# Performance work log

Hardware: AMD Instinct MI355X
Metric: run time of the kernel (lower is better)

## Reference

```python
import jax, jax.numpy as jnp
import numpy as np

K = 32
EPS = 1e-16


def setup_inputs() -> dict:
    key = jax.random.key(0)
    k1, k2, k3 = jax.random.split(key, 3)
    N_l, N_h, D, F = 8192, 32768, 3, 128
    x = jax.random.normal(k1, (N_l, F), dtype=jnp.float32)
    pos_l = jax.random.normal(k2, (N_l, D), dtype=jnp.float32)
    pos_h = jax.random.normal(k3, (N_h, D), dtype=jnp.float32)
    return {"x": x, "pos_l": pos_l, "pos_h": pos_h}


def reference(x, pos_l, pos_h):
    # Squared pairwise distances [N_h, N_l] via ||h||^2 - 2 h.l + ||l||^2
    h2 = jnp.sum(pos_h * pos_h, axis=1, keepdims=True)        # [N_h, 1]
    l2 = jnp.sum(pos_l * pos_l, axis=1)                        # [N_l]
    d2 = h2 - 2.0 * (pos_h @ pos_l.T) + l2[None, :]            # [N_h, N_l]
    # k nearest source points per target point
    neg_d2k, idx = jax.lax.top_k(-d2, K)                       # [N_h, K]
    d2k = -neg_d2k
    # Inverse squared-distance weights (torch_geometric: 1/clamp(d2, min=1e-16))
    w = 1.0 / jnp.maximum(d2k, EPS)                            # [N_h, K]
    xk = x[idx]                                                # [N_h, K, F]
    y = jnp.einsum('nk,nkf->nf', w, xk) / jnp.sum(w, axis=1, keepdims=True)
    return y
```

## Files before the change

kernel.cpp:

```cpp
#include <hip/hip_runtime.h>
#include <stdint.h>

#define NL      8192
#define NH      32768
#define FDIM    128
#define KSEL    32
#define QPW     8
#define NWAVES  4
#define BLOCK   (NWAVES * 64)
#define QPB     (NWAVES * QPW)
#define BUFCAP  256
#define NGROUP  (NL / 64)
#define NCELL   4096
#define TSCAN   4
#define MAXPASS 6

__device__ __forceinline__ int imin(int a, int b) { return a < b ? a : b; }
__device__ __forceinline__ int imax(int a, int b) { return a > b ? a : b; }

__device__ __forceinline__ uint32_t spread3(uint32_t x) {
    x &= 0xFu;
    x = (x | (x << 16)) & 0x030000FFu;
    x = (x | (x << 8))  & 0x0300F00Fu;
    x = (x | (x << 4))  & 0x030C30C3u;
    x = (x | (x << 2))  & 0x09249249u;
    return x;
}
__device__ __forceinline__ int cell_of(float px, float py, float pz) {
    int ix = (int)floorf((px + 4.0f) * 2.0f);
    int iy = (int)floorf((py + 4.0f) * 2.0f);
    int iz = (int)floorf((pz + 4.0f) * 2.0f);
    ix = imin(imax(ix, 0), 15); iy = imin(imax(iy, 0), 15); iz = imin(imax(iz, 0), 15);
    return (int)(spread3((uint32_t)ix) | (spread3((uint32_t)iy) << 1) | (spread3((uint32_t)iz) << 2));
}

__global__ void k_cell_count(const float* __restrict__ pos_l, int* __restrict__ hist) {
    const int i = blockIdx.x * 256 + threadIdx.x;
    if (i >= NL) return;
    const int c = cell_of(pos_l[i * 3 + 0], pos_l[i * 3 + 1], pos_l[i * 3 + 2]);
    atomicAdd(&hist[c], 1);
}

__global__ void k_cell_scan(const int* __restrict__ hist, int* __restrict__ cursor) {
    __shared__ int part[256];
    __shared__ int partpref[256];
    const int tid = threadIdx.x;
    int loc[16];
    int s = 0;
#pragma unroll
    for (int i = 0; i < 16; ++i) { loc[i] = s; s += hist[tid * 16 + i]; }
    part[tid] = s;
    __syncthreads();
    if (tid == 0) {
        int a = 0;
        for (int t = 0; t < 256; ++t) { partpref[t] = a; a += part[t]; }
    }
    __syncthreads();
    const int b = partpref[tid];
#pragma unroll
    for (int i = 0; i < 16; ++i) cursor[tid * 16 + i] = b + loc[i];
}

__global__ void k_scatter(const float* __restrict__ pos_l, int* __restrict__ cursor,
                          float4* __restrict__ sorted, int* __restrict__ oidx) {
    const int i = blockIdx.x * 256 + threadIdx.x;
    if (i >= NL) return;
    const float px = pos_l[i * 3 + 0];
    const float py = pos_l[i * 3 + 1];
    const float pz = pos_l[i * 3 + 2];
    const int c = cell_of(px, py, pz);
    const int pos = atomicAdd(&cursor[c], 1);
    sorted[pos] = make_float4(px, py, pz, px * px + py * py + pz * pz);
    oidx[pos] = i;
}

__global__ void k_spheres(const float4* __restrict__ sorted, float4* __restrict__ spheres) {
    const int g = blockIdx.x;
    const int lane = threadIdx.x;
    const float4 p = sorted[g * 64 + lane];
    float sx = p.x, sy = p.y, sz = p.z;
#pragma unroll
    for (int j = 32; j >= 1; j >>= 1) {
        sx += __shfl_xor(sx, j); sy += __shfl_xor(sy, j); sz += __shfl_xor(sz, j);
    }
    const float cx = sx * (1.0f / 64.0f), cy = sy * (1.0f / 64.0f), cz = sz * (1.0f / 64.0f);
    const float dx = p.x - cx, dy = p.y - cy, dz = p.z - cz;
    float d2 = dx * dx + dy * dy + dz * dz;
#pragma unroll
    for (int j = 32; j >= 1; j >>= 1) d2 = fmaxf(d2, __shfl_xor(d2, j));
    if (lane == 0) spheres[g] = make_float4(cx, cy, cz, sqrtf(d2) + 1e-3f);
}

__global__ __launch_bounds__(BLOCK, 4)
void knn_interp_kernel(const float* __restrict__ x,
                       const float* __restrict__ pos_h,
                       const float4* __restrict__ sorted,
                       const float4* __restrict__ spheres,
                       const int* __restrict__ oidx,
                       float* __restrict__ out)
{
    __shared__ float4   s_grp[NGROUP];
    __shared__ unsigned long long s_surv[NWAVES][QPW][2];
    __shared__ uint16_t s_idx[QPB][BUFCAP];
    __shared__ float    s_w[QPB][KSEL];
    __shared__ int      s_wi[QPB][KSEL];

    const int tid   = threadIdx.x;
    const int lane  = tid & 63;
    const int wid   = tid >> 6;
    const int qbase = blockIdx.x * QPB + wid * QPW;
    const unsigned long long mlt = (1ull << lane) - 1ull;

    if (tid < NGROUP) s_grp[tid] = spheres[tid];
    __syncthreads();

    const float4 cA = s_grp[lane];
    const float4 cB = s_grp[lane + 64];

    float qx[QPW], qy[QPW], qz[QPW], h2q[QPW], tauD[QPW];

#pragma unroll
    for (int q = 0; q < QPW; ++q) {
        const int gq = qbase + q;
        qx[q] = pos_h[gq * 3 + 0];
        qy[q] = pos_h[gq * 3 + 1];
        qz[q] = pos_h[gq * 3 + 2];
        h2q[q] = fmaf(qx[q], qx[q], fmaf(qy[q], qy[q], qz[q] * qz[q]));

        const float dAx = qx[q] - cA.x, dAy = qy[q] - cA.y, dAz = qz[q] - cA.z;
        const float dA  = fmaf(dAx, dAx, fmaf(dAy, dAy, dAz * dAz));
        const float dBx = qx[q] - cB.x, dBy = qy[q] - cB.y, dBz = qz[q] - cB.z;
        const float dB  = fmaf(dBx, dBx, fmaf(dBy, dBy, dBz * dBz));

        int kA = (int)((__float_as_uint(dA) & 0xFFFFFF00u) | (uint32_t)lane);
        int kB = (int)((__float_as_uint(dB) & 0xFFFFFF00u) | (uint32_t)(lane + 64));

        int gsel[TSCAN];
#pragma unroll
        for (int t = 0; t < TSCAN; ++t) {
            int m = imin(kA, kB);
#pragma unroll
            for (int j = 1; j <= 32; j <<= 1) m = imin(m, __shfl_xor(m, j));
            gsel[t] = m & 0xFF;
            if (kA == m) kA = 0x7FFFFFFF;
            if (kB == m) kB = 0x7FFFFFFF;
        }

        float dmin = INFINITY;
#pragma unroll
        for (int t = 0; t < TSCAN; ++t) {
            const float4 p = sorted[(gsel[t] << 6) + lane];
            const float s = fmaf(qx[q], p.x, fmaf(qy[q], p.y, qz[q] * p.z));
            dmin = fminf(dmin, fmaf(-2.0f, s, p.w));
        }
        float v = dmin;
#pragma unroll
        for (int k = 2; k <= 64; k <<= 1) {
#pragma unroll
            for (int j = k >> 1; j >= 1; j >>= 1) {
                const float o     = __shfl_xor(v, j);
                const bool  up    = ((lane & k) == 0);
                const bool  lower = ((lane & j) == 0);
                v = (lower == up) ? fminf(v, o) : fmaxf(v, o);
            }
        }
        const float tau = __shfl(v, 31) + 1e-4f;
        tauD[q] = tau;

        const float st = sqrtf(fmaxf(tau + h2q[q], 0.0f)) + 1e-3f;
        const float tA = st + cA.w, tB = st + cB.w;
        const unsigned long long bA = __ballot(dA <= tA * tA);
        const unsigned long long bB = __ballot(dB <= tB * tB);
        if (lane == 0) { s_surv[wid][q][0] = bA; s_surv[wid][q][1] = bB; }
    }

#pragma unroll 1
    for (int q = 0; q < QPW; ++q) {
        const int QQ = wid * QPW + q;
        const int gq = qbase + q;
        float tau = tauD[q];
        int M = 0;

#pragma unroll 1
        for (int pass = 0; pass < MAXPASS; ++pass) {
            M = 0;
#pragma unroll 1
            for (int h = 0; h < 2; ++h) {
                unsigned long long mm = s_surv[wid][q][h];
                while (mm) {
                    const int g = (h << 6) + __builtin_ctzll(mm);
                    mm &= mm - 1;
                    const float4 p = sorted[(g << 6) + lane];
                    const float s = fmaf(qx[q], p.x, fmaf(qy[q], p.y, qz[q] * p.z));
                    const float D = fmaf(-2.0f, s, p.w);
                    const bool hit = (D <= tau);
                    const unsigned long long b = __ballot(hit);
                    if (b) {
                        const int o = M + (int)__popcll(b & mlt);
                        if (hit && o < BUFCAP) s_idx[QQ][o] = (uint16_t)((g << 6) + lane);
                        M += (int)__popcll(b);
                    }
                }
            }
            if (M <= BUFCAP) break;
            int kk[4];
#pragma unroll
            for (int r = 0; r < 4; ++r) {
                const int idx = (int)s_idx[QQ][64 * r + lane];
                const float4 c = sorted[idx];
                const float s = fmaf(qx[q], c.x, fmaf(qy[q], c.y, qz[q] * c.z));
                const float d2 = fmaxf(fmaf(-2.0f, s, c.w) + h2q[q], 0.0f);
                kk[r] = __float_as_int(d2);
            }
            int lo = 0, hi = 0x7F800000;
            while (lo < hi) {
                const int mid = (int)(((unsigned)lo + (unsigned)hi) >> 1);
                int cnt = 0;
#pragma unroll
                for (int r = 0; r < 4; ++r)
                    cnt += (int)__popcll(__ballot(kk[r] <= mid));
                if (cnt >= KSEL) hi = mid; else lo = mid + 1;
            }
            tau = __int_as_float(lo) - h2q[q] + 1e-4f;
        }
        if (M > BUFCAP) M = BUFCAP;

        const double ax = (double)qx[q], ay = (double)qy[q], az = (double)qz[q];
        if (M <= 128) {
            const int i0 = (2 * lane     < M) ? (int)s_idx[QQ][2 * lane]     : -1;
            const int i1 = (2 * lane + 1 < M) ? (int)s_idx[QQ][2 * lane + 1] : -1;
            float f0 = INFINITY, f1 = INFINITY;
            if (i0 >= 0) {
                const float4 c = sorted[i0];
                const double dx = (double)c.x - ax, dy = (double)c.y - ay, dz = (double)c.z - az;
                f0 = (float)(dx * dx + dy * dy + dz * dz);
            }
            if (i1 >= 0) {
                const float4 c = sorted[i1];
                const double dx = (double)c.x - ax, dy = (double)c.y - ay, dz = (double)c.z - az;
                f1 = (float)(dx * dx + dy * dy + dz * dz);
            }
            int v0 = __float_as_int(f0);
            int v1 = __float_as_int(f1);
#pragma unroll
            for (int k = 2; k <= 128; k <<= 1) {
                const bool up = ((lane & (k >> 1)) == 0);
#pragma unroll
                for (int j = k >> 1; j >= 2; j >>= 1) {
                    const int  xo    = j >> 1;
                    const bool lower = ((lane & xo) == 0);
                    const int o0 = __shfl_xor(v0, xo);
                    const int o1 = __shfl_xor(v1, xo);
                    v0 = (lower == up) ? imin(v0, o0) : imax(v0, o0);
                    v1 = (lower == up) ? imin(v1, o1) : imax(v1, o1);
                }
                const int mn = imin(v0, v1), mx = imax(v0, v1);
                v0 = up ? mn : mx;
                v1 = up ? mx : mn;
            }
            const int tau32 = __shfl(v1, 15);
            const bool a0 = (i0 >= 0) && (__float_as_int(f0) <= tau32);
            const bool a1 = (i1 >= 0) && (__float_as_int(f1) <= tau32);
            const unsigned long long b0 = __ballot(a0);
            const unsigned long long b1 = __ballot(a1);
            const int base = (int)__popcll(b0 & mlt) + (int)__popcll(b1 & mlt);
            const int p0 = base;
            const int p1 = base + (a0 ? 1 : 0);
            if (a0 && p0 < KSEL) { s_w[QQ][p0] = 1.0f / fmaxf(f0, 1e-16f); s_wi[QQ][p0] = oidx[i0]; }
            if (a1 && p1 < KSEL) { s_w[QQ][p1] = 1.0f / fmaxf(f1, 1e-16f); s_wi[QQ][p1] = oidx[i1]; }
        } else {
            int ii[4]; float ff[4]; int kk_[4];
#pragma unroll
            for (int r = 0; r < 4; ++r) {
                const int e = 4 * lane + r;
                ii[r] = (e < M) ? (int)s_idx[QQ][e] : -1;
                ff[r] = INFINITY;
                if (ii[r] >= 0) {
                    const float4 c = sorted[ii[r]];
                    const double dx = (double)c.x - ax, dy = (double)c.y - ay, dz = (double)c.z - az;
                    ff[r] = (float)(dx * dx + dy * dy + dz * dz);
                }
                kk_[r] = __float_as_int(ff[r]);
            }
            int lo = 0, hi = 0x7F800000;
            while (lo < hi) {
                const int mid = (int)(((unsigned)lo + (unsigned)hi) >> 1);
                int cnt = 0;
#pragma unroll
                for (int r = 0; r < 4; ++r)
                    cnt += (int)__popcll(__ballot(ii[r] >= 0 && kk_[r] <= mid));
                if (cnt >= KSEL) hi = mid; else lo = mid + 1;
            }
            const int tau32 = lo;
            bool a[4]; unsigned long long b[4];
#pragma unroll
            for (int r = 0; r < 4; ++r) {
                a[r] = (ii[r] >= 0) && (kk_[r] <= tau32);
                b[r] = __ballot(a[r]);
            }
            int base = 0;
#pragma unroll
            for (int r = 0; r < 4; ++r) base += (int)__popcll(b[r] & mlt);
            int pref = 0;
#pragma unroll
            for (int r = 0; r < 4; ++r) {
                const int p = base + pref;
                if (a[r] && p < KSEL) { s_w[QQ][p] = 1.0f / fmaxf(ff[r], 1e-16f); s_wi[QQ][p] = oidx[ii[r]]; }
                pref += (a[r] ? 1 : 0);
            }
        }

        float acc0 = 0.0f, acc1 = 0.0f, wsum = 0.0f;
#pragma unroll 8
        for (int t = 0; t < KSEL; ++t) {
            const float w   = s_w[QQ][t];
            const int   idx = s_wi[QQ][t];
            const float* row = x + (size_t)idx * FDIM;
            acc0 = fmaf(w, row[lane], acc0);
            acc1 = fmaf(w, row[lane + 64], acc1);
            wsum += w;
        }
        const float invw = 1.0f / wsum;
        out[(size_t)gq * FDIM + lane]      = acc0 * invw;
        out[(size_t)gq * FDIM + 64 + lane] = acc1 * invw;
    }
}

extern "C" void kernel_launch(void* const* d_in, const int* in_sizes, int n_in,
                              void* d_out, int out_size, void* d_ws, size_t ws_size,
                              hipStream_t stream) {
    const float* x     = (const float*)d_in[0];
    const float* pos_l = (const float*)d_in[1];
    const float* pos_h = (const float*)d_in[2];
    float* out = (float*)d_out;

    char* ws = (char*)d_ws;
    int*    hist    = (int*)(ws + 0);
    int*    cursor  = (int*)(ws + 16384);
    float4* spheres = (float4*)(ws + 32768);
    float4* sorted  = (float4*)(ws + 65536);
    int*    oidx    = (int*)(ws + 65536 + 131072);

    hipMemsetAsync(hist, 0, NCELL * sizeof(int), stream);
    hipLaunchKernelGGL(k_cell_count, dim3(NL / 256), dim3(256), 0, stream, pos_l, hist);
    hipLaunchKernelGGL(k_cell_scan, dim3(1), dim3(256), 0, stream, hist, cursor);
    hipLaunchKernelGGL(k_scatter, dim3(NL / 256), dim3(256), 0, stream, pos_l, cursor, sorted, oidx);
    hipLaunchKernelGGL(k_spheres, dim3(NGROUP), dim3(64), 0, stream, sorted, spheres);
    hipLaunchKernelGGL(knn_interp_kernel, dim3(NH / QPB), dim3(BLOCK), 0, stream,
                       x, pos_h, sorted, spheres, oidx, out);
}
```

Before: 220.9 us.

## Fuse preprocessing into one kernel, shrink blocks, use ballot rank-select and prefetch

The memset and four preprocessing kernels (histogram, scan, scatter, sphere bounds) are merged into one single-block kernel that does its counting sort in shared memory, removing several launches. The main kernel moves to smaller blocks (2 waves, 4 queries each) with a higher occupancy hint, and reads sphere data straight from global memory instead of staging it in LDS. Bitonic sorts and iterative min-extraction are replaced by a ballot-based binary-search rank select. The initial threshold now takes the 32nd smallest of 64 lane minima rather than the sorted value at lane 31. The candidate scan loop prefetches the next group's points to hide load latency. The single-block preprocess serialises that stage on one CU, and the binary search adds about 31 ballot rounds per selection.

```diff
diff --git a/kernel.cpp b/kernel.cpp
--- a/kernel.cpp
+++ b/kernel.cpp
@@ -5,8 +5,8 @@
 #define NH      32768
 #define FDIM    128
 #define KSEL    32
-#define QPW     8
-#define NWAVES  4
+#define QPW     4
+#define NWAVES  2
 #define BLOCK   (NWAVES * 64)
 #define QPB     (NWAVES * QPW)
 #define BUFCAP  256
@@ -14,9 +14,42 @@
 #define NCELL   4096
 #define TSCAN   4
 #define MAXPASS 6
+#define PRE_T   1024
 
 __device__ __forceinline__ int imin(int a, int b) { return a < b ? a : b; }
 __device__ __forceinline__ int imax(int a, int b) { return a > b ? a : b; }
+
+__device__ __forceinline__ int rank_select1(int k0, int rank) {
+    unsigned lo = 0u, hi = 0x7F800000u;
+    while (lo < hi) {
+        const int mid = (int)((lo + hi) >> 1);
+        const int cnt = (int)__popcll(__ballot(k0 <= mid));
+        if (cnt >= rank) hi = (unsigned)mid; else lo = (unsigned)mid + 1u;
+    }
+    return (int)lo;
+}
+__device__ __forceinline__ int rank_select2(int k0, int k1, int rank) {
+    unsigned lo = 0u, hi = 0x7F800000u;
+    while (lo < hi) {
+        const int mid = (int)((lo + hi) >> 1);
+        const int cnt = (int)__popcll(__ballot(k0 <= mid))
+                      + (int)__popcll(__ballot(k1 <= mid));
+        if (cnt >= rank) hi = (unsigned)mid; else lo = (unsigned)mid + 1u;
+    }
+    return (int)lo;
+}
+__device__ __forceinline__ int rank_select4(const int* k, int rank) {
+    unsigned lo = 0u, hi = 0x7F800000u;
+    while (lo < hi) {
+        const int mid = (int)((lo + hi) >> 1);
+        int cnt = 0;
+#pragma unroll
+        for (int r = 0; r < 4; ++r)
+            cnt += (int)__popcll(__ballot(k[r] <= mid));
+        if (cnt >= rank) hi = (unsigned)mid; else lo = (unsigned)mid + 1u;
+    }
+    return (int)lo;
+}
 
 __device__ __forceinline__ uint32_t spread3(uint32_t x) {
     x &= 0xFu;
@@ -34,64 +67,78 @@
     return (int)(spread3((uint32_t)ix) | (spread3((uint32_t)iy) << 1) | (spread3((uint32_t)iz) << 2));
 }
 
-__global__ void k_cell_count(const float* __restrict__ pos_l, int* __restrict__ hist) {
-    const int i = blockIdx.x * 256 + threadIdx.x;
-    if (i >= NL) return;
-    const int c = cell_of(pos_l[i * 3 + 0], pos_l[i * 3 + 1], pos_l[i * 3 + 2]);
-    atomicAdd(&hist[c], 1);
-}
-
-__global__ void k_cell_scan(const int* __restrict__ hist, int* __restrict__ cursor) {
-    __shared__ int part[256];
-    __shared__ int partpref[256];
-    const int tid = threadIdx.x;
-    int loc[16];
-    int s = 0;
-#pragma unroll
-    for (int i = 0; i < 16; ++i) { loc[i] = s; s += hist[tid * 16 + i]; }
-    part[tid] = s;
-    __syncthreads();
-    if (tid == 0) {
-        int a = 0;
-        for (int t = 0; t < 256; ++t) { partpref[t] = a; a += part[t]; }
-    }
-    __syncthreads();
-    const int b = partpref[tid];
-#pragma unroll
-    for (int i = 0; i < 16; ++i) cursor[tid * 16 + i] = b + loc[i];
-}
-
-__global__ void k_scatter(const float* __restrict__ pos_l, int* __restrict__ cursor,
-                          float4* __restrict__ sorted, int* __restrict__ oidx) {
-    const int i = blockIdx.x * 256 + threadIdx.x;
-    if (i >= NL) return;
-    const float px = pos_l[i * 3 + 0];
-    const float py = pos_l[i * 3 + 1];
-    const float pz = pos_l[i * 3 + 2];
-    const int c = cell_of(px, py, pz);
-    const int pos = atomicAdd(&cursor[c], 1);
-    sorted[pos] = make_float4(px, py, pz, px * px + py * py + pz * pz);
-    oidx[pos] = i;
-}
-
-__global__ void k_spheres(const float4* __restrict__ sorted, float4* __restrict__ spheres) {
-    const int g = blockIdx.x;
-    const int lane = threadIdx.x;
-    const float4 p = sorted[g * 64 + lane];
-    float sx = p.x, sy = p.y, sz = p.z;
-#pragma unroll
-    for (int j = 32; j >= 1; j >>= 1) {
-        sx += __shfl_xor(sx, j); sy += __shfl_xor(sy, j); sz += __shfl_xor(sz, j);
-    }
-    const float cx = sx * (1.0f / 64.0f), cy = sy * (1.0f / 64.0f), cz = sz * (1.0f / 64.0f);
-    const float dx = p.x - cx, dy = p.y - cy, dz = p.z - cz;
-    float d2 = dx * dx + dy * dy + dz * dz;
-#pragma unroll
-    for (int j = 32; j >= 1; j >>= 1) d2 = fmaxf(d2, __shfl_xor(d2, j));
-    if (lane == 0) spheres[g] = make_float4(cx, cy, cz, sqrtf(d2) + 1e-3f);
-}
-
-__global__ __launch_bounds__(BLOCK, 4)
+__global__ __launch_bounds__(PRE_T)
+void k_preprocess(const float* __restrict__ pos_l,
+                  float4* __restrict__ sorted, int* __restrict__ oidx,
+                  float4* __restrict__ spheres)
+{
+    __shared__ int hist[NCELL];
+    __shared__ int wpart[PRE_T / 64];
+    const int tid  = threadIdx.x;
+    const int lane = tid & 63;
+    const int wv   = tid >> 6;
+
+    for (int i = tid; i < NCELL; i += PRE_T) hist[i] = 0;
+    __syncthreads();
+
+    int cc[8]; float px[8], py[8], pz[8];
+#pragma unroll
+    for (int r = 0; r < 8; ++r) {
+        const int i = r * PRE_T + tid;
+        px[r] = pos_l[i * 3 + 0];
+        py[r] = pos_l[i * 3 + 1];
+        pz[r] = pos_l[i * 3 + 2];
+        cc[r] = cell_of(px[r], py[r], pz[r]);
+        atomicAdd(&hist[cc[r]], 1);
+    }
+    __syncthreads();
+
+    int loc[4]; int ts = 0;
+#pragma unroll
+    for (int i = 0; i < 4; ++i) { loc[i] = ts; ts += hist[tid * 4 + i]; }
+    int incl = ts;
+#pragma unroll
+    for (int d = 1; d < 64; d <<= 1) {
+        const int t = __shfl_up(incl, d);
+        if (lane >= d) incl += t;
+    }
+    if (lane == 63) wpart[wv] = incl;
+    __syncthreads();
+    int base = 0;
+    for (int j = 0; j < wv; ++j) base += wpart[j];
+    const int texcl = base + incl - ts;
+#pragma unroll
+    for (int i = 0; i < 4; ++i) hist[tid * 4 + i] = texcl + loc[i];
+    __syncthreads();
+
+#pragma unroll
+    for (int r = 0; r < 8; ++r) {
+        const int pos = atomicAdd(&hist[cc[r]], 1);
+        sorted[pos] = make_float4(px[r], py[r], pz[r],
+                                  fmaf(px[r], px[r], fmaf(py[r], py[r], pz[r] * pz[r])));
+        oidx[pos] = r * PRE_T + tid;
+    }
+    __syncthreads();
+
+#pragma unroll
+    for (int r = 0; r < NGROUP / (PRE_T / 64); ++r) {
+        const int g = wv * (NGROUP / (PRE_T / 64)) + r;
+        const float4 p = sorted[g * 64 + lane];
+        float sx = p.x, sy = p.y, sz = p.z;
+#pragma unroll
+        for (int j = 32; j >= 1; j >>= 1) {
+            sx += __shfl_xor(sx, j); sy += __shfl_xor(sy, j); sz += __shfl_xor(sz, j);
+        }
+        const float cx = sx * (1.0f / 64.0f), cy = sy * (1.0f / 64.0f), cz = sz * (1.0f / 64.0f);
+        const float dx = p.x - cx, dy = p.y - cy, dz = p.z - cz;
+        float d2 = fmaf(dx, dx, fmaf(dy, dy, dz * dz));
+#pragma unroll
+        for (int j = 32; j >= 1; j >>= 1) d2 = fmaxf(d2, __shfl_xor(d2, j));
+        if (lane == 0) spheres[g] = make_float4(cx, cy, cz, sqrtf(d2) + 1e-3f);
+    }
+}
+
+__global__ __launch_bounds__(BLOCK, 6)
 void knn_interp_kernel(const float* __restrict__ x,
                        const float* __restrict__ pos_h,
                        const float4* __restrict__ sorted,
@@ -99,11 +146,10 @@
                        const int* __restrict__ oidx,
                        float* __restrict__ out)
 {
-    __shared__ float4   s_grp[NGROUP];
-    __shared__ unsigned long long s_surv[NWAVES][QPW][2];
     __shared__ uint16_t s_idx[QPB][BUFCAP];
     __shared__ float    s_w[QPB][KSEL];
     __shared__ int      s_wi[QPB][KSEL];
+    __shared__ unsigned long long s_surv[NWAVES][QPW][2];
 
     const int tid   = threadIdx.x;
     const int lane  = tid & 63;
@@ -111,63 +157,47 @@
     const int qbase = blockIdx.x * QPB + wid * QPW;
     const unsigned long long mlt = (1ull << lane) - 1ull;
 
-    if (tid < NGROUP) s_grp[tid] = spheres[tid];
-    __syncthreads();
-
-    const float4 cA = s_grp[lane];
-    const float4 cB = s_grp[lane + 64];
+    const float4 cA = spheres[lane];
+    const float4 cB = spheres[lane + 64];
 
     float qx[QPW], qy[QPW], qz[QPW], h2q[QPW], tauD[QPW];
 
 #pragma unroll
     for (int q = 0; q < QPW; ++q) {
         const int gq = qbase + q;
-        qx[q] = pos_h[gq * 3 + 0];
-        qy[q] = pos_h[gq * 3 + 1];
-        qz[q] = pos_h[gq * 3 + 2];
-        h2q[q] = fmaf(qx[q], qx[q], fmaf(qy[q], qy[q], qz[q] * qz[q]));
-
-        const float dAx = qx[q] - cA.x, dAy = qy[q] - cA.y, dAz = qz[q] - cA.z;
+        const float ax = pos_h[gq * 3 + 0];
+        const float ay = pos_h[gq * 3 + 1];
+        const float az = pos_h[gq * 3 + 2];
+        qx[q] = ax; qy[q] = ay; qz[q] = az;
+        const float h2 = fmaf(ax, ax, fmaf(ay, ay, az * az));
+        h2q[q] = h2;
+
+        const float dAx = ax - cA.x, dAy = ay - cA.y, dAz = az - cA.z;
         const float dA  = fmaf(dAx, dAx, fmaf(dAy, dAy, dAz * dAz));
-        const float dBx = qx[q] - cB.x, dBy = qy[q] - cB.y, dBz = qz[q] - cB.z;
+        const float dBx = ax - cB.x, dBy = ay - cB.y, dBz = az - cB.z;
         const float dB  = fmaf(dBx, dBx, fmaf(dBy, dBy, dBz * dBz));
 
-        int kA = (int)((__float_as_uint(dA) & 0xFFFFFF00u) | (uint32_t)lane);
-        int kB = (int)((__float_as_uint(dB) & 0xFFFFFF00u) | (uint32_t)(lane + 64));
-
-        int gsel[TSCAN];
-#pragma unroll
+        const int kA = (int)((__float_as_uint(dA) & 0xFFFFFF00u) | (uint32_t)lane);
+        const int kB = (int)((__float_as_uint(dB) & 0xFFFFFF00u) | (uint32_t)(lane + 64));
+        const int t4 = rank_select2(kA, kB, TSCAN);
+        unsigned long long gm0 = __ballot(kA <= t4);
+        unsigned long long gm1 = __ballot(kB <= t4);
+
+        float dmin = INFINITY;
+#pragma unroll 1
         for (int t = 0; t < TSCAN; ++t) {
-            int m = imin(kA, kB);
-#pragma unroll
-            for (int j = 1; j <= 32; j <<= 1) m = imin(m, __shfl_xor(m, j));
-            gsel[t] = m & 0xFF;
-            if (kA == m) kA = 0x7FFFFFFF;
-            if (kB == m) kB = 0x7FFFFFFF;
-        }
-
-        float dmin = INFINITY;
-#pragma unroll
-        for (int t = 0; t < TSCAN; ++t) {
-            const float4 p = sorted[(gsel[t] << 6) + lane];
-            const float s = fmaf(qx[q], p.x, fmaf(qy[q], p.y, qz[q] * p.z));
+            int g;
+            if (gm0) { g = __builtin_ctzll(gm0); gm0 &= gm0 - 1ull; }
+            else     { g = 64 + __builtin_ctzll(gm1); gm1 &= gm1 - 1ull; }
+            const float4 p = sorted[(g << 6) + lane];
+            const float s = fmaf(ax, p.x, fmaf(ay, p.y, az * p.z));
             dmin = fminf(dmin, fmaf(-2.0f, s, p.w));
         }
-        float v = dmin;
-#pragma unroll
-        for (int k = 2; k <= 64; k <<= 1) {
-#pragma unroll
-            for (int j = k >> 1; j >= 1; j >>= 1) {
-                const float o     = __shfl_xor(v, j);
-                const bool  up    = ((lane & k) == 0);
-                const bool  lower = ((lane & j) == 0);
-                v = (lower == up) ? fminf(v, o) : fmaxf(v, o);
-            }
-        }
-        const float tau = __shfl(v, 31) + 1e-4f;
-        tauD[q] = tau;
-
-        const float st = sqrtf(fmaxf(tau + h2q[q], 0.0f)) + 1e-3f;
+        const float d2min = fmaxf(dmin + h2, 0.0f);
+        const int t32 = rank_select1(__float_as_int(d2min), KSEL);
+        const float tau_d2 = __int_as_float(t32) + 1e-4f;
+        tauD[q] = tau_d2 - h2;
+        const float st = sqrtf(tau_d2) + 1e-3f;
         const float tA = st + cA.w, tB = st + cB.w;
         const unsigned long long bA = __ballot(dA <= tA * tA);
         const unsigned long long bB = __ballot(dB <= tB * tB);
@@ -178,29 +208,38 @@
     for (int q = 0; q < QPW; ++q) {
         const int QQ = wid * QPW + q;
         const int gq = qbase + q;
+        const float ax = qx[q], ay = qy[q], az = qz[q];
         float tau = tauD[q];
         int M = 0;
 
 #pragma unroll 1
         for (int pass = 0; pass < MAXPASS; ++pass) {
             M = 0;
+            unsigned long long m0 = s_surv[wid][q][0];
+            unsigned long long m1 = s_surv[wid][q][1];
+            int g_cur = -1;
+            if (m0)      { g_cur = __builtin_ctzll(m0); m0 &= m0 - 1ull; }
+            else if (m1) { g_cur = 64 + __builtin_ctzll(m1); m1 &= m1 - 1ull; }
+            float4 pc = make_float4(0, 0, 0, 0);
+            if (g_cur >= 0) pc = sorted[(g_cur << 6) + lane];
 #pragma unroll 1
-            for (int h = 0; h < 2; ++h) {
-                unsigned long long mm = s_surv[wid][q][h];
-                while (mm) {
-                    const int g = (h << 6) + __builtin_ctzll(mm);
-                    mm &= mm - 1;
-                    const float4 p = sorted[(g << 6) + lane];
-                    const float s = fmaf(qx[q], p.x, fmaf(qy[q], p.y, qz[q] * p.z));
-                    const float D = fmaf(-2.0f, s, p.w);
-                    const bool hit = (D <= tau);
-                    const unsigned long long b = __ballot(hit);
-                    if (b) {
-                        const int o = M + (int)__popcll(b & mlt);
-                        if (hit && o < BUFCAP) s_idx[QQ][o] = (uint16_t)((g << 6) + lane);
-                        M += (int)__popcll(b);
-                    }
+            while (g_cur >= 0) {
+                int g_nxt = -1;
+                if (m0)      { g_nxt = __builtin_ctzll(m0); m0 &= m0 - 1ull; }
+                else if (m1) { g_nxt = 64 + __builtin_ctzll(m1); m1 &= m1 - 1ull; }
+                float4 pn = pc;
+                if (g_nxt >= 0) pn = sorted[(g_nxt << 6) + lane];
+
+                const float s = fmaf(ax, pc.x, fmaf(ay, pc.y, az * pc.z));
+                const float D = fmaf(-2.0f, s, pc.w);
+                const bool hit = (D <= tau);
+                const unsigned long long b = __ballot(hit);
+                if (b) {
+                    const int o = M + (int)__popcll(b & mlt);
+                    if (hit && o < BUFCAP) s_idx[QQ][o] = (uint16_t)((g_cur << 6) + lane);
+                    M += (int)__popcll(b);
                 }
+                g_cur = g_nxt; pc = pn;
             }
             if (M <= BUFCAP) break;
             int kk[4];
@@ -208,59 +247,34 @@
             for (int r = 0; r < 4; ++r) {
                 const int idx = (int)s_idx[QQ][64 * r + lane];
                 const float4 c = sorted[idx];
-                const float s = fmaf(qx[q], c.x, fmaf(qy[q], c.y, qz[q] * c.z));
+                const float s = fmaf(ax, c.x, fmaf(ay, c.y, az * c.z));
                 const float d2 = fmaxf(fmaf(-2.0f, s, c.w) + h2q[q], 0.0f);
                 kk[r] = __float_as_int(d2);
             }
-            int lo = 0, hi = 0x7F800000;
-            while (lo < hi) {
-                const int mid = (int)(((unsigned)lo + (unsigned)hi) >> 1);
-                int cnt = 0;
-#pragma unroll
-                for (int r = 0; r < 4; ++r)
-                    cnt += (int)__popcll(__ballot(kk[r] <= mid));
-                if (cnt >= KSEL) hi = mid; else lo = mid + 1;
-            }
-            tau = __int_as_float(lo) - h2q[q] + 1e-4f;
+            const int tk = rank_select4(kk, KSEL);
+            tau = __int_as_float(tk) + 1e-4f - h2q[q];
         }
         if (M > BUFCAP) M = BUFCAP;
 
-        const double ax = (double)qx[q], ay = (double)qy[q], az = (double)qz[q];
+        const double axd = (double)ax, ayd = (double)ay, azd = (double)az;
         if (M <= 128) {
             const int i0 = (2 * lane     < M) ? (int)s_idx[QQ][2 * lane]     : -1;
             const int i1 = (2 * lane + 1 < M) ? (int)s_idx[QQ][2 * lane + 1] : -1;
             float f0 = INFINITY, f1 = INFINITY;
             if (i0 >= 0) {
                 const float4 c = sorted[i0];
-                const double dx = (double)c.x - ax, dy = (double)c.y - ay, dz = (double)c.z - az;
+                const double dx = (double)c.x - axd, dy = (double)c.y - ayd, dz = (double)c.z - azd;
                 f0 = (float)(dx * dx + dy * dy + dz * dz);
             }
             if (i1 >= 0) {
                 const float4 c = sorted[i1];
-                const double dx = (double)c.x - ax, dy = (double)c.y - ay, dz = (double)c.z - az;
+                const double dx = (double)c.x - axd, dy = (double)c.y - ayd, dz = (double)c.z - azd;
                 f1 = (float)(dx * dx + dy * dy + dz * dz);
             }
-            int v0 = __float_as_int(f0);
-            int v1 = __float_as_int(f1);
-#pragma unroll
-            for (int k = 2; k <= 128; k <<= 1) {
-                const bool up = ((lane & (k >> 1)) == 0);
-#pragma unroll
-                for (int j = k >> 1; j >= 2; j >>= 1) {
-                    const int  xo    = j >> 1;
-                    const bool lower = ((lane & xo) == 0);
-                    const int o0 = __shfl_xor(v0, xo);
-                    const int o1 = __shfl_xor(v1, xo);
-                    v0 = (lower == up) ? imin(v0, o0) : imax(v0, o0);
-                    v1 = (lower == up) ? imin(v1, o1) : imax(v1, o1);
-                }
-                const int mn = imin(v0, v1), mx = imax(v0, v1);
-                v0 = up ? mn : mx;
-                v1 = up ? mx : mn;
-            }
-            const int tau32 = __shfl(v1, 15);
-            const bool a0 = (i0 >= 0) && (__float_as_int(f0) <= tau32);
-            const bool a1 = (i1 >= 0) && (__float_as_int(f1) <= tau32);
+            const int k0 = __float_as_int(f0), k1 = __float_as_int(f1);
+            const int tau32 = rank_select2(k0, k1, KSEL);
+            const bool a0 = (i0 >= 0) && (k0 <= tau32);
+            const bool a1 = (i1 >= 0) && (k1 <= tau32);
             const unsigned long long b0 = __ballot(a0);
             const unsigned long long b1 = __ballot(a1);
             const int base = (int)__popcll(b0 & mlt) + (int)__popcll(b1 & mlt);
@@ -277,21 +291,12 @@
                 ff[r] = INFINITY;
                 if (ii[r] >= 0) {
                     const float4 c = sorted[ii[r]];
-                    const double dx = (double)c.x - ax, dy = (double)c.y - ay, dz = (double)c.z - az;
+                    const double dx = (double)c.x - axd, dy = (double)c.y - ayd, dz = (double)c.z - azd;
                     ff[r] = (float)(dx * dx + dy * dy + dz * dz);
                 }
                 kk_[r] = __float_as_int(ff[r]);
             }
-            int lo = 0, hi = 0x7F800000;
-            while (lo < hi) {
-                const int mid = (int)(((unsigned)lo + (unsigned)hi) >> 1);
-                int cnt = 0;
-#pragma unroll
-                for (int r = 0; r < 4; ++r)
-                    cnt += (int)__popcll(__ballot(ii[r] >= 0 && kk_[r] <= mid));
-                if (cnt >= KSEL) hi = mid; else lo = mid + 1;
-            }
-            const int tau32 = lo;
+            const int tau32 = rank_select4(kk_, KSEL);
             bool a[4]; unsigned long long b[4];
 #pragma unroll
             for (int r = 0; r < 4; ++r) {
@@ -335,17 +340,12 @@
     float* out = (float*)d_out;
 
     char* ws = (char*)d_ws;
-    int*    hist    = (int*)(ws + 0);
-    int*    cursor  = (int*)(ws + 16384);
-    float4* spheres = (float4*)(ws + 32768);
-    float4* sorted  = (float4*)(ws + 65536);
-    int*    oidx    = (int*)(ws + 65536 + 131072);
-
-    hipMemsetAsync(hist, 0, NCELL * sizeof(int), stream);
-    hipLaunchKernelGGL(k_cell_count, dim3(NL / 256), dim3(256), 0, stream, pos_l, hist);
-    hipLaunchKernelGGL(k_cell_scan, dim3(1), dim3(256), 0, stream, hist, cursor);
-    hipLaunchKernelGGL(k_scatter, dim3(NL / 256), dim3(256), 0, stream, pos_l, cursor, sorted, oidx);
-    hipLaunchKernelGGL(k_spheres, dim3(NGROUP), dim3(64), 0, stream, sorted, spheres);
+    float4* sorted  = (float4*)(ws + 0);
+    int*    oidx    = (int*)(ws + 131072);
+    float4* spheres = (float4*)(ws + 163840);
+
+    hipLaunchKernelGGL(k_preprocess, dim3(1), dim3(PRE_T), 0, stream,
+                       pos_l, sorted, oidx, spheres);
     hipLaunchKernelGGL(knn_interp_kernel, dim3(NH / QPB), dim3(BLOCK), 0, stream,
                        x, pos_h, sorted, spheres, oidx, out);
 }
```

New measurement: 246.4 us. +11.6%, slower.
